# Optimization experiments

Measured on AMD Instinct MI355X. Metric: run time of the kernel, lower is better.

The kernel has to match this reference:

```python
import jax, jax.numpy as jnp
import numpy as np

N, E, F_IN, D, X_DIM, T_DIM = 5000, 80000, 32, 64, 3, 6
P1, P2, H = 256, 32, 256
LOG_SCALE = 1.4763057  # sqrt(c) * 1.4763057 with c=1; Euclidean logmap0 is identity
W_DATA, W_PDE, W_ENT = 1.0, 1.0, 1.0

def time_encode(t):
    k_lin = T_DIM // 2
    k_log = T_DIM - k_lin
    s_lin = 10.0 ** jnp.arange(2, 2 * T_DIM, 1, dtype=jnp.float32)
    s_log = 10.0 ** jnp.arange(-2, 2 * T_DIM, 1, dtype=jnp.float32)
    t_lin = (t / jnp.clip(s_lin, 1e-7))[:k_lin]
    t_log = jnp.log((t / jnp.clip(s_log, 1e-7))[:k_log] + 1.0)
    return jnp.concatenate([t_lin, t_log])

def _forward(x0, adj, t, y, W_enc, W_pool1, W_pool2, W_emb1, W_emb2, W1, b1, W2, b2):
    t0 = t[0]
    # ---- encode: encoder + Euclidean log-map scaling ----
    z_x = jnp.tanh(x0 @ W_enc)                      # [N, D+X_DIM]
    z = z_x[:, :-X_DIM] * LOG_SCALE                 # [N, D]
    x_sp = 0.0 * z_x[:, -X_DIM:]                    # eps = 0 as in encode()
    t_enc = time_encode(t0)                         # [T_DIM]
    tx = jnp.concatenate([t_enc[None, :] * jnp.ones((N, 1)), x_sp], axis=-1)  # [N, T_DIM+X_DIM]
    # ---- renorm: dense adjacency scatter + DiffPool-style coarsening ----
    A = jnp.zeros((N, N), dtype=x0.dtype).at[adj[0], adj[1]].set(1.0)
    x = z
    y_cur = y                                        # [1, N]
    z_r = z
    y_r = y
    loss_ent = 0.0
    for Wp, We in ((W_pool1, W_emb1), (W_pool2, W_emb2)):
        S = jax.nn.softmax((x @ Wp) * LOG_SCALE, axis=0)        # [m, n] soft assignment
        m, n = S.shape
        ze = jnp.tanh(A @ (x @ We))                             # GNN embed at this level
        x = jnp.einsum('ij,ik->jk', S, ze) * (n / m)            # pooled features [n, D]
        y_cur = jnp.einsum('ij,ki->kj', S, y_cur) * (n / m)     # pooled targets [1, n]
        A = jnp.einsum('ji,jk,kl->il', S, A, S)                 # S^T A S -> [n, n]
        z_r = jnp.concatenate([z_r, x], axis=0)
        y_r = jnp.concatenate([y_r, y_cur], axis=-1)
        loss_ent = loss_ent + jax.scipy.special.entr(S).mean()
    M = z_r.shape[0]                                 # N + P1 + P2
    tx_all = tx[0] * jnp.ones((M, 1))                # broadcast first row -> [M, T_DIM+X_DIM]
    # ---- decoder + val_grad_lap: nested jacfwd Hessian diagonal ----
    def decode(txz):
        h = jnp.tanh(txz @ W1 + b1)
        return h @ W2 + b2                           # [1]
    def vgl(tx_i, z_i):
        def f(tx_):
            u = decode(jnp.concatenate([tx_, z_i]))
            return u, u
        def vg(tx_):
            g, u = jax.jacfwd(f, has_aux=True)(tx_)
            return g, (g, u)
        g2, (g, u) = jax.jacfwd(vg, has_aux=True)(tx_i)  # [1, d, d]
        hess = jax.vmap(jnp.diag)(g2)                     # [1, d]
        lap = hess[:, 1:].sum(1)                          # [1]
        return u, g, lap
    u, grad, lap = jax.vmap(vgl)(tx_all, z_r)        # [M,1], [M,1,d], [M,1]
    red = u.sum(-1)                                   # reduction -> [M]
    loss_data = jnp.mean(jnp.square(red - y_r[0]))
    res = grad[:, 0, 0] - lap[:, 0]                   # heat-equation residual u_t - lap
    loss_pde = jnp.mean(jnp.square(res))
    return W_DATA * loss_data + W_PDE * loss_pde + W_ENT * loss_ent

def setup_inputs():
    key = jax.random.key(0)
    ks = jax.random.split(key, 13)
    d_tx = T_DIM + X_DIM
    return {
        'x0': jax.random.normal(ks[0], (N, F_IN), dtype=jnp.float32),
        'adj': jax.random.randint(ks[1], (2, E), 0, N),
        't': jax.random.uniform(ks[2], (1,), dtype=jnp.float32) * 100.0,
        'y': jax.random.normal(ks[3], (1, N), dtype=jnp.float32),
        'W_enc': 0.2 * jax.random.normal(ks[4], (F_IN, D + X_DIM), dtype=jnp.float32),
        'W_pool1': 0.2 * jax.random.normal(ks[5], (D, P1), dtype=jnp.float32),
        'W_pool2': 0.2 * jax.random.normal(ks[6], (D, P2), dtype=jnp.float32),
        'W_emb1': 0.1 * jax.random.normal(ks[7], (D, D), dtype=jnp.float32),
        'W_emb2': 0.1 * jax.random.normal(ks[8], (D, D), dtype=jnp.float32),
        'W1': 0.1 * jax.random.normal(ks[9], (d_tx + D, H), dtype=jnp.float32),
        'b1': 0.01 * jax.random.normal(ks[10], (H,), dtype=jnp.float32),
        'W2': 0.1 * jax.random.normal(ks[11], (H, 1), dtype=jnp.float32),
        'b2': jnp.zeros((1,), dtype=jnp.float32),
    }

def reference(x0, adj, t, y, W_enc, W_pool1, W_pool2, W_emb1, W_emb2, W1, b1, W2, b2):
    return _forward(x0, adj, t, y, W_enc, W_pool1, W_pool2, W_emb1, W_emb2, W1, b1, W2, b2)
```

## Files before the change

kernel.cpp:

```cpp
#include <hip/hip_runtime.h>
#include <math.h>

#define NN 5000
#define EE 80000
#define FIN 32
#define DD 64
#define XD 3
#define TD 6
#define PP1 256
#define PP2 32
#define HH 256
#define MM (NN + PP1 + PP2)
#define CAP 64
#define NTILES 79
#define LOG_SCALE 1.4763057f
#define Y2SCALE (256.f / 5000.f)

#define A2CH 40
#define X2CH 79

#define ACC_OFF   0u
#define CNT_OFF   64u
#define DEG_OFF   256u
#define Y2A_OFF   20256u
#define X2_OFF    21280u
#define A2_OFF    86816u
#define BM_OFF    348960u
#define ZERO_BYTES 3473960u
#define PART_OFF  348960u
#define XW2_OFF   760608u
#define S2_OFF    826144u
#define ZE2_OFF   858912u
#define X3_OFF    924448u
#define Y3_OFF    932640u
#define BUCK_OFF  3473984u
#define ZEP_OFF   4753984u
#define Z_OFF     6033984u
#define S1_OFF    7313984u
#define AS1_OFF   12433984u
#define CQ_OFF    17553984u
#define DRES_OFF  17556032u
#define PA2_OFF   17598336u
#define PX2_OFF   28084096u
#define WS_ROOMY  33261504u

__device__ __forceinline__ float bsum256(float v, float* red) {
    int t = threadIdx.x;
    red[t] = v; __syncthreads();
    #pragma unroll
    for (int o = 128; o > 0; o >>= 1) {
        if (t < o) red[t] += red[t + o];
        __syncthreads();
    }
    float r = red[0]; __syncthreads();
    return r;
}

__global__ __launch_bounds__(256) void stage0(
        const float* __restrict__ x0, const float* __restrict__ Wenc,
        float* __restrict__ z,
        const int* __restrict__ adj, unsigned int* __restrict__ mask,
        int* __restrict__ bucket, int* __restrict__ deg,
        const float* __restrict__ t, const float* __restrict__ W1,
        const float* __restrict__ b1, float* __restrict__ cq) {
    __shared__ float smem[FIN * DD + 4 * FIN];
    int b = blockIdx.x;
    int tid = threadIdx.x;
    if (b < 1250) {
        float (*wx)[DD] = (float(*)[DD])smem;
        float (*xr)[FIN] = (float(*)[FIN])(smem + FIN * DD);
        int i0 = b << 2;
        int j = tid & 63;
        #pragma unroll
        for (int m = 0; m < 8; ++m) {
            int k = (tid >> 6) + (m << 2);
            wx[k][j] = Wenc[k * (DD + XD) + j];
        }
        if (tid < 128) xr[tid >> 5][tid & 31] = x0[(i0 + (tid >> 5)) * FIN + (tid & 31)];
        __syncthreads();
        int r = tid >> 6;
        float s = 0.f;
        #pragma unroll
        for (int k = 0; k < FIN; ++k) s = fmaf(xr[r][k], wx[k][j], s);
        z[(i0 + r) * DD + j] = tanhf(s) * LOG_SCALE;
    } else if (b < 1563) {
        int e = (b - 1250) * 256 + tid;
        if (e < EE) {
            int i = adj[e], jj = adj[EE + e];
            unsigned int key = (unsigned int)(i * NN + jj);
            unsigned int bit = 1u << (key & 31u);
            unsigned int old = atomicOr(&mask[key >> 5], bit);
            if (!(old & bit)) {
                int slot = atomicAdd(&deg[i], 1);
                if (slot < CAP) bucket[i * CAP + slot] = jj;
            }
        }
    } else {
        float* te = smem;
        int h = tid;
        if (h == 0) {
            float t0 = t[0];
            te[0] = t0 / 1e2f;
            te[1] = t0 / 1e3f;
            te[2] = t0 / 1e4f;
            te[3] = logf(t0 * 100.f + 1.f);
            te[4] = logf(t0 * 10.f + 1.f);
            te[5] = logf(t0 + 1.f);
        }
        __syncthreads();
        float c = b1[h];
        #pragma unroll
        for (int j2 = 0; j2 < TD; ++j2) c = fmaf(te[j2], W1[j2 * HH + h], c);
        float q = 0.f;
        #pragma unroll
        for (int j2 = 1; j2 < TD + XD; ++j2) { float w = W1[j2 * HH + h]; q = fmaf(w, w, q); }
        cq[h] = c;
        cq[HH + h] = q;
    }
}

__global__ __launch_bounds__(256) void stage1(
        const float* __restrict__ z, const float* __restrict__ Wp1,
        float* __restrict__ S1, float* __restrict__ part,
        const int* __restrict__ bucket, const int* __restrict__ deg,
        const float* __restrict__ We1, float* __restrict__ zep) {
    __shared__ float smem[2 * 64 * 64];
    int b = blockIdx.x;
    int tid = threadIdx.x;
    if (b < NTILES * 4) {
        float (*sa)[64] = (float(*)[64])smem;
        float (*sb)[64] = (float(*)[64])(smem + 4096);
        int tm = (b >> 2) << 6;
        int tn = (b & 3) << 6;
        int r0 = tid >> 4, c0 = (tid & 15) << 2;
        const float4 zero4 = make_float4(0.f, 0.f, 0.f, 0.f);
        #pragma unroll
        for (int m = 0; m < 4; ++m) {
            int row = r0 + (m << 4);
            int gr = tm + row;
            *(float4*)&sa[row][c0] = (gr < NN) ? *(const float4*)&z[gr * DD + c0] : zero4;
            *(float4*)&sb[row][c0] = *(const float4*)&Wp1[row * PP1 + tn + c0];
        }
        __syncthreads();
        int tx = (tid & 15) << 2;
        int ty = (tid >> 4) << 2;
        float acc[4][4] = {};
        #pragma unroll
        for (int kk = 0; kk < 64; ++kk) {
            float a0 = sa[ty + 0][kk];
            float a1 = sa[ty + 1][kk];
            float a2 = sa[ty + 2][kk];
            float a3 = sa[ty + 3][kk];
            float4 bv = *(const float4*)&sb[kk][tx];
            acc[0][0] = fmaf(a0, bv.x, acc[0][0]);
            acc[0][1] = fmaf(a0, bv.y, acc[0][1]);
            acc[0][2] = fmaf(a0, bv.z, acc[0][2]);
            acc[0][3] = fmaf(a0, bv.w, acc[0][3]);
            acc[1][0] = fmaf(a1, bv.x, acc[1][0]);
            acc[1][1] = fmaf(a1, bv.y, acc[1][1]);
            acc[1][2] = fmaf(a1, bv.z, acc[1][2]);
            acc[1][3] = fmaf(a1, bv.w, acc[1][3]);
            acc[2][0] = fmaf(a2, bv.x, acc[2][0]);
            acc[2][1] = fmaf(a2, bv.y, acc[2][1]);
            acc[2][2] = fmaf(a2, bv.z, acc[2][2]);
            acc[2][3] = fmaf(a2, bv.w, acc[2][3]);
            acc[3][0] = fmaf(a3, bv.x, acc[3][0]);
            acc[3][1] = fmaf(a3, bv.y, acc[3][1]);
            acc[3][2] = fmaf(a3, bv.z, acc[3][2]);
            acc[3][3] = fmaf(a3, bv.w, acc[3][3]);
        }
        #pragma unroll
        for (int i2 = 0; i2 < 4; ++i2)
            #pragma unroll
            for (int j = 0; j < 4; ++j) acc[i2][j] *= LOG_SCALE;
        #pragma unroll
        for (int i2 = 0; i2 < 4; ++i2) {
            int gr = tm + ty + i2;
            if (gr < NN)
                *(float4*)&S1[gr * PP1 + tn + tx] =
                    make_float4(acc[i2][0], acc[i2][1], acc[i2][2], acc[i2][3]);
        }
        int nvalid = NN - (tm + ty);
        nvalid = (nvalid < 0) ? 0 : (nvalid > 4 ? 4 : nvalid);
        float vm[4], vs[4];
        #pragma unroll
        for (int j = 0; j < 4; ++j) {
            float m = -3.0e38f;
            #pragma unroll
            for (int i2 = 0; i2 < 4; ++i2) if (i2 < nvalid) m = fmaxf(m, acc[i2][j]);
            float s = 0.f;
            #pragma unroll
            for (int i2 = 0; i2 < 4; ++i2) if (i2 < nvalid) s += expf(acc[i2][j] - m);
            vm[j] = m; vs[j] = s;
        }
        __syncthreads();
        float* redm = smem;
        float* reds = smem + 1024;
        int g = tid >> 4;
        #pragma unroll
        for (int j = 0; j < 4; ++j) {
            redm[g * 64 + tx + j] = vm[j];
            reds[g * 64 + tx + j] = vs[j];
        }
        __syncthreads();
        if (tid < 64) {
            float M = -3.0e38f, S = 0.f;
            #pragma unroll
            for (int g2 = 0; g2 < 16; ++g2) {
                float m2 = redm[g2 * 64 + tid], s2 = reds[g2 * 64 + tid];
                float Mn = fmaxf(M, m2);
                S = S * expf(M - Mn) + s2 * expf(m2 - Mn);
                M = Mn;
            }
            int rt = tm >> 6;
            part[rt * 512 + tn + tid] = M;
            part[rt * 512 + 256 + tn + tid] = S;
        }
    } else {
        float (*zs)[DD] = (float(*)[DD])smem;
        int w = tid >> 6, d = tid & 63;
        int i = ((b - NTILES * 4) << 2) + w;
        int n = min(deg[i], CAP);
        const int* bk = bucket + i * CAP;
        float a0 = 0.f, a1 = 0.f, a2 = 0.f, a3 = 0.f;
        int s = 0;
        for (; s + 4 <= n; s += 4) {
            a0 += z[bk[s] * DD + d];
            a1 += z[bk[s + 1] * DD + d];
            a2 += z[bk[s + 2] * DD + d];
            a3 += z[bk[s + 3] * DD + d];
        }
        for (; s < n; ++s) a0 += z[bk[s] * DD + d];
        zs[w][d] = (a0 + a1) + (a2 + a3);
        __syncthreads();
        float acc = 0.f;
        #pragma unroll
        for (int k = 0; k < DD; ++k) acc = fmaf(zs[w][k], We1[k * DD + d], acc);
        zep[i * DD + d] = tanhf(acc);
    }
}

__global__ void smax_norm(float* __restrict__ S, const float* __restrict__ part,
                          const float* __restrict__ y, float* __restrict__ y2acc,
                          float* __restrict__ ent) {
    __shared__ float red[256];
    __shared__ float ybuf[4][64];
    __shared__ float cst[64];
    int rt = blockIdx.x % NTILES, ct = blockIdx.x / NTILES;
    int lc = threadIdx.x & 63, q = threadIdx.x >> 6;
    int c = (ct << 6) + lc;
    float M = -3.0e38f, Sv = 0.f;
    for (int ch = q; ch < NTILES; ch += 4) {
        float m2 = part[ch * 512 + c];
        float s2 = part[ch * 512 + 256 + c];
        float Mn = fmaxf(M, m2);
        Sv = Sv * expf(M - Mn) + s2 * expf(m2 - Mn);
        M = Mn;
    }
    red[threadIdx.x] = M; ybuf[q][lc] = Sv;
    __syncthreads();
    if (q == 0) {
        float Mm = red[lc], Ss = ybuf[0][lc];
        #pragma unroll
        for (int g = 1; g < 4; ++g) {
            float m2 = red[g * 64 + lc], s2 = ybuf[g][lc];
            float Mn = fmaxf(Mm, m2);
            Ss = Ss * expf(Mm - Mn) + s2 * expf(m2 - Mn);
            Mm = Mn;
        }
        cst[lc] = Mm + logf(Ss);
    }
    __syncthreads();
    float mxlns = cst[lc];
    float en = 0.f, ys = 0.f;
    #pragma unroll
    for (int k = 0; k < 16; ++k) {
        int r = (rt << 6) + (k << 2) + q;
        if (r < NN) {
            float v = S[r * PP1 + c];
            float s = expf(v - mxlns);
            S[r * PP1 + c] = s;
            en += s * (mxlns - v);
            ys = fmaf(s, y[r], ys);
        }
    }
    __syncthreads();
    ybuf[q][lc] = ys;
    en = bsum256(en, red);
    if (threadIdx.x == 0) atomicAdd(ent, en);
    if (q == 0) atomicAdd(&y2acc[c], ybuf[0][lc] + ybuf[1][lc] + ybuf[2][lc] + ybuf[3][lc]);
}

__global__ void gather_as(const int* __restrict__ bucket, const int* __restrict__ deg,
                          const float* __restrict__ S1, float* __restrict__ AS1) {
    int i = blockIdx.x, c = threadIdx.x;
    int n = min(deg[i], CAP);
    const int* bk = bucket + i * CAP;
    float a0 = 0.f, a1 = 0.f, a2 = 0.f, a3 = 0.f;
    int s = 0;
    for (; s + 4 <= n; s += 4) {
        a0 += S1[bk[s] * PP1 + c];
        a1 += S1[bk[s + 1] * PP1 + c];
        a2 += S1[bk[s + 2] * PP1 + c];
        a3 += S1[bk[s + 3] * PP1 + c];
    }
    for (; s < n; ++s) a0 += S1[bk[s] * PP1 + c];
    AS1[i * PP1 + c] = (a0 + a1) + (a2 + a3);
}

__global__ __launch_bounds__(256) void gemm_fused(
        const float* __restrict__ S1, const float* __restrict__ AS1,
        const float* __restrict__ zep, float* __restrict__ PA2, float* __restrict__ PX2) {
    __shared__ float sa[32][64];
    __shared__ float sb[32][64];
    int b = blockIdx.x;
    const float* B;
    float* dst;
    int tm, tn, k0, k1, NB;
    if (b < 640) {
        int tile = b & 15, chunk = b >> 4;
        tm = (tile >> 2) << 6; tn = (tile & 3) << 6;
        k0 = chunk * 128; k1 = min(k0 + 128, NN);
        B = AS1; NB = PP1;
        dst = PA2 + chunk * (PP1 * PP1);
    } else {
        int b2 = b - 640;
        int tile = b2 & 3, chunk = b2 >> 2;
        tm = tile << 6; tn = 0;
        k0 = chunk * 64; k1 = min(k0 + 64, NN);
        B = zep; NB = DD;
        dst = PX2 + chunk * (PP1 * DD);
    }
    int tid = threadIdx.x;
    int tx = (tid & 15) << 2;
    int ty = (tid >> 4) << 2;
    int r0 = tid >> 4, c0 = (tid & 15) << 2;
    int r1 = (tid + 256) >> 4, c1 = c0;
    float acc[4][4] = {};
    const float4 z4 = make_float4(0.f, 0.f, 0.f, 0.f);
    for (int kb = k0; kb < k1; kb += 32) {
        int ka0 = kb + r0, ka1 = kb + r1;
        *(float4*)&sa[r0][c0] = (ka0 < k1) ? *(const float4*)&S1[ka0 * PP1 + tm + c0] : z4;
        *(float4*)&sa[r1][c1] = (ka1 < k1) ? *(const float4*)&S1[ka1 * PP1 + tm + c1] : z4;
        *(float4*)&sb[r0][c0] = (ka0 < k1) ? *(const float4*)&B[ka0 * NB + tn + c0] : z4;
        *(float4*)&sb[r1][c1] = (ka1 < k1) ? *(const float4*)&B[ka1 * NB + tn + c1] : z4;
        __syncthreads();
        #pragma unroll
        for (int kk = 0; kk < 32; ++kk) {
            float4 av = *(const float4*)&sa[kk][ty];
            float4 bv = *(const float4*)&sb[kk][tx];
            acc[0][0] = fmaf(av.x, bv.x, acc[0][0]);
            acc[0][1] = fmaf(av.x, bv.y, acc[0][1]);
            acc[0][2] = fmaf(av.x, bv.z, acc[0][2]);
            acc[0][3] = fmaf(av.x, bv.w, acc[0][3]);
            acc[1][0] = fmaf(av.y, bv.x, acc[1][0]);
            acc[1][1] = fmaf(av.y, bv.y, acc[1][1]);
            acc[1][2] = fmaf(av.y, bv.z, acc[1][2]);
            acc[1][3] = fmaf(av.y, bv.w, acc[1][3]);
            acc[2][0] = fmaf(av.z, bv.x, acc[2][0]);
            acc[2][1] = fmaf(av.z, bv.y, acc[2][1]);
            acc[2][2] = fmaf(av.z, bv.z, acc[2][2]);
            acc[2][3] = fmaf(av.z, bv.w, acc[2][3]);
            acc[3][0] = fmaf(av.w, bv.x, acc[3][0]);
            acc[3][1] = fmaf(av.w, bv.y, acc[3][1]);
            acc[3][2] = fmaf(av.w, bv.z, acc[3][2]);
            acc[3][3] = fmaf(av.w, bv.w, acc[3][3]);
        }
        __syncthreads();
    }
    #pragma unroll
    for (int i = 0; i < 4; ++i)
        *(float4*)&dst[(tm + ty + i) * NB + tn + tx] =
            make_float4(acc[i][0], acc[i][1], acc[i][2], acc[i][3]);
}

__global__ void reduce_parts(const float* __restrict__ PA2, const float* __restrict__ PX2,
                             float* __restrict__ A2, float* __restrict__ x2) {
    int idx = blockIdx.x * 256 + threadIdx.x;
    if (idx < PP1 * PP1) {
        float s = 0.f;
        #pragma unroll 8
        for (int c = 0; c < A2CH; ++c) s += PA2[c * (PP1 * PP1) + idx];
        A2[idx] = s;
    } else {
        int e = idx - PP1 * PP1;
        float s = 0.f;
        #pragma unroll 8
        for (int c = 0; c < X2CH; ++c) s += PX2[c * (PP1 * DD) + e];
        x2[e] = s * Y2SCALE;
    }
}

__global__ void gemm_tn(const float* __restrict__ A, const float* __restrict__ B,
                        float* __restrict__ C, int M, int N, int K, int kchunk, float scale) {
    __shared__ float sa[32][64];
    __shared__ float sb[32][64];
    int tilesN = N >> 6;
    int tm = (blockIdx.x / tilesN) << 6;
    int tn = (blockIdx.x % tilesN) << 6;
    int k0 = blockIdx.y * kchunk;
    int k1 = min(k0 + kchunk, K);
    int tid = threadIdx.x;
    int tx = (tid & 15) << 2;
    int ty = (tid >> 4) << 2;
    float acc[4][4] = {};
    for (int kb = k0; kb < k1; kb += 32) {
        #pragma unroll
        for (int t = 0; t < 8; ++t) {
            int idx = tid + (t << 8);
            int r = idx >> 6, cc = idx & 63;
            int k = kb + r;
            sa[r][cc] = (k < k1) ? A[k * M + tm + cc] : 0.f;
            sb[r][cc] = (k < k1) ? B[k * N + tn + cc] : 0.f;
        }
        __syncthreads();
        #pragma unroll
        for (int kk = 0; kk < 32; ++kk) {
            float4 av = *(const float4*)&sa[kk][ty];
            float4 bv = *(const float4*)&sb[kk][tx];
            acc[0][0] = fmaf(av.x, bv.x, acc[0][0]);
            acc[0][1] = fmaf(av.x, bv.y, acc[0][1]);
            acc[0][2] = fmaf(av.x, bv.z, acc[0][2]);
            acc[0][3] = fmaf(av.x, bv.w, acc[0][3]);
            acc[1][0] = fmaf(av.y, bv.x, acc[1][0]);
            acc[1][1] = fmaf(av.y, bv.y, acc[1][1]);
            acc[1][2] = fmaf(av.y, bv.z, acc[1][2]);
            acc[1][3] = fmaf(av.y, bv.w, acc[1][3]);
            acc[2][0] = fmaf(av.z, bv.x, acc[2][0]);
            acc[2][1] = fmaf(av.z, bv.y, acc[2][1]);
            acc[2][2] = fmaf(av.z, bv.z, acc[2][2]);
            acc[2][3] = fmaf(av.z, bv.w, acc[2][3]);
            acc[3][0] = fmaf(av.w, bv.x, acc[3][0]);
            acc[3][1] = fmaf(av.w, bv.y, acc[3][1]);
            acc[3][2] = fmaf(av.w, bv.z, acc[3][2]);
            acc[3][3] = fmaf(av.w, bv.w, acc[3][3]);
        }
        __syncthreads();
    }
    #pragma unroll
    for (int i = 0; i < 4; ++i)
        #pragma unroll
        for (int j = 0; j < 4; ++j)
            atomicAdd(&C[(tm + ty + i) * N + tn + tx + j], acc[i][j] * scale);
}

__global__ void mm2_fused(const float* __restrict__ x2, const float* __restrict__ We2,
                          const float* __restrict__ Wp2, float* __restrict__ XW2,
                          float* __restrict__ S2) {
    int gid = blockIdx.x * 256 + threadIdx.x;
    if (gid < PP1 * DD) {
        int i = gid >> 6, j = gid & 63;
        float s = 0.f;
        #pragma unroll
        for (int k = 0; k < DD; ++k) s = fmaf(x2[i * DD + k], We2[k * DD + j], s);
        XW2[gid] = s;
    } else {
        int e = gid - PP1 * DD;
        int i = e >> 5, j = e & 31;
        float s = 0.f;
        #pragma unroll
        for (int k = 0; k < DD; ++k) s = fmaf(x2[i * DD + k], Wp2[k * PP2 + j], s);
        S2[e] = s * LOG_SCALE;
    }
}

__global__ void level2b(float* __restrict__ S2, float* __restrict__ ent,
                        const float* __restrict__ y2acc, float* __restrict__ y3,
                        const float* __restrict__ A2, const float* __restrict__ XW2,
                        float* __restrict__ ze2) {
    __shared__ float red[256];
    int t = threadIdx.x;
    if (blockIdx.x < PP2) {
        int p = blockIdx.x;
        float l = S2[t * PP2 + p];
        red[t] = l; __syncthreads();
        #pragma unroll
        for (int o = 128; o > 0; o >>= 1) {
            if (t < o) red[t] = fmaxf(red[t], red[t + o]);
            __syncthreads();
        }
        float mx = red[0]; __syncthreads();
        float ex = expf(l - mx);
        float sum = bsum256(ex, red);
        float lns = logf(sum), inv = 1.f / sum;
        float s = ex * inv;
        S2[t * PP2 + p] = s;
        float en = s * (mx + lns - l);
        float ys = s * y2acc[t];
        en = bsum256(en, red);
        ys = bsum256(ys, red);
        if (t == 0) {
            atomicAdd(ent, en);
            y3[p] = ys * ((32.f / 256.f) * Y2SCALE);
        }
    } else {
        int gid = (blockIdx.x - PP2) * 256 + t;
        int i = gid >> 6, j = gid & 63;
        const float* a = A2 + i * PP1;
        float s = 0.f;
        #pragma unroll 16
        for (int k = 0; k < PP1; ++k) s = fmaf(a[k], XW2[k * DD + j], s);
        ze2[gid] = tanhf(s);
    }
}

__global__ void pool_x3(const float* __restrict__ S2, const float* __restrict__ ze2,
                        float* __restrict__ x3) {
    __shared__ float pr[4][64];
    int j = blockIdx.x;
    int d = threadIdx.x & 63, q = threadIdx.x >> 6;
    float a = 0.f;
    #pragma unroll 4
    for (int i = q * 64; i < q * 64 + 64; ++i)
        a = fmaf(S2[i * PP2 + j], ze2[i * DD + d], a);
    pr[q][d] = a;
    __syncthreads();
    if (q == 0) x3[j * DD + d] = (pr[0][d] + pr[1][d] + pr[2][d] + pr[3][d]) * (32.f / 256.f);
}

__global__ __launch_bounds__(256) void decoder8(
        const float* __restrict__ z, const float* __restrict__ x2,
        const float* __restrict__ x3, const float* __restrict__ y,
        const float* __restrict__ y2acc, const float* __restrict__ y3,
        const float* __restrict__ W1, const float* __restrict__ W2,
        const float* __restrict__ b2, const float* __restrict__ cq,
        float* __restrict__ dres, int* __restrict__ cnt,
        const float* __restrict__ acc, float* __restrict__ out) {
    __shared__ float zr[8][DD];
    __shared__ float rw[8][3][4];
    __shared__ int lastflag;
    int t = threadIdx.x;
    int i0 = blockIdx.x << 3;
    #pragma unroll
    for (int e = t; e < 512; e += 256) {
        int r = e >> 6, d = e & 63;
        int i = i0 + r;
        float v;
        if (i < NN) v = z[i * DD + d];
        else if (i < NN + PP1) v = x2[(i - NN) * DD + d];
        else v = x3[(i - NN - PP1) * DD + d];
        zr[r][d] = v;
    }
    __syncthreads();
    int h = t;
    float c0 = cq[h];
    float a[8];
    #pragma unroll
    for (int r = 0; r < 8; ++r) a[r] = c0;
    #pragma unroll 8
    for (int k = 0; k < DD; ++k) {
        float w = W1[(TD + XD + k) * HH + h];
        #pragma unroll
        for (int r = 0; r < 8; ++r) a[r] = fmaf(zr[r][k], w, a[r]);
    }
    float w2h = W2[h], w1h = W1[h], qh = cq[HH + h];
    float pu[8], pg[8], pl[8];
    #pragma unroll
    for (int r = 0; r < 8; ++r) {
        float th = tanhf(a[r]);
        float g1 = 1.f - th * th;
        pu[r] = w2h * th;
        pg[r] = w2h * g1 * w1h;
        pl[r] = w2h * (-2.f * th * g1) * qh;
    }
    #pragma unroll
    for (int o = 32; o > 0; o >>= 1) {
        #pragma unroll
        for (int r = 0; r < 8; ++r) {
            pu[r] += __shfl_xor(pu[r], o);
            pg[r] += __shfl_xor(pg[r], o);
            pl[r] += __shfl_xor(pl[r], o);
        }
    }
    int wave = t >> 6, lane = t & 63;
    if (lane == 0) {
        #pragma unroll
        for (int r = 0; r < 8; ++r) {
            rw[r][0][wave] = pu[r];
            rw[r][1][wave] = pg[r];
            rw[r][2][wave] = pl[r];
        }
    }
    __syncthreads();
    if (t < 8) {
        int r = t, i = i0 + r;
        float su = rw[r][0][0] + rw[r][0][1] + rw[r][0][2] + rw[r][0][3];
        float sg = rw[r][1][0] + rw[r][1][1] + rw[r][1][2] + rw[r][1][3];
        float sl = rw[r][2][0] + rw[r][2][1] + rw[r][2][2] + rw[r][2][3];
        float u = su + b2[0];
        float yv = (i < NN) ? y[i]
                 : (i < NN + PP1) ? y2acc[i - NN] * Y2SCALE
                 : y3[i - NN - PP1];
        float du = u - yv;
        float res = sg - sl;
        dres[i * 2] = du * du;
        dres[i * 2 + 1] = res * res;
        __threadfence();
    }
    __syncthreads();
    if (t == 0) lastflag = atomicAdd(cnt, 1);
    __syncthreads();
    if (lastflag == (MM / 8) - 1) {
        __threadfence();
        float* red = (float*)zr;
        float sd = 0.f, sp = 0.f;
        for (int i = t; i < MM; i += 256) {
            sd += dres[i * 2];
            sp += dres[i * 2 + 1];
        }
        sd = bsum256(sd, red);
        sp = bsum256(sp, red);
        if (t == 0)
            out[0] = sd * (1.f / MM) + sp * (1.f / MM)
                   + acc[2] * (1.f / (float)(NN * PP1)) + acc[3] * (1.f / (float)(PP1 * PP2));
    }
}

extern "C" void kernel_launch(void* const* d_in, const int* in_sizes, int n_in,
                              void* d_out, int out_size, void* d_ws, size_t ws_size,
                              hipStream_t stream) {
    const float* x0   = (const float*)d_in[0];
    const int*   adj  = (const int*)d_in[1];
    const float* t    = (const float*)d_in[2];
    const float* y    = (const float*)d_in[3];
    const float* Wenc = (const float*)d_in[4];
    const float* Wp1  = (const float*)d_in[5];
    const float* Wp2  = (const float*)d_in[6];
    const float* We1  = (const float*)d_in[7];
    const float* We2  = (const float*)d_in[8];
    const float* W1   = (const float*)d_in[9];
    const float* b1   = (const float*)d_in[10];
    const float* W2   = (const float*)d_in[11];
    const float* b2   = (const float*)d_in[12];

    char* ws = (char*)d_ws;
    float* acc   = (float*)(ws + ACC_OFF);
    int*   cnt   = (int*)(ws + CNT_OFF);
    int*   deg   = (int*)(ws + DEG_OFF);
    float* y2acc = (float*)(ws + Y2A_OFF);
    float* x2    = (float*)(ws + X2_OFF);
    float* A2    = (float*)(ws + A2_OFF);
    unsigned int* mask = (unsigned int*)(ws + BM_OFF);
    float* part  = (float*)(ws + PART_OFF);
    float* XW2   = (float*)(ws + XW2_OFF);
    float* S2    = (float*)(ws + S2_OFF);
    float* ze2   = (float*)(ws + ZE2_OFF);
    float* x3    = (float*)(ws + X3_OFF);
    float* y3    = (float*)(ws + Y3_OFF);
    int*   buck  = (int*)(ws + BUCK_OFF);
    float* zep   = (float*)(ws + ZEP_OFF);
    float* z     = (float*)(ws + Z_OFF);
    float* S1    = (float*)(ws + S1_OFF);
    float* AS1   = (float*)(ws + AS1_OFF);
    float* cq    = (float*)(ws + CQ_OFF);
    float* dres  = (float*)(ws + DRES_OFF);
    float* PA2   = (float*)(ws + PA2_OFF);
    float* PX2   = (float*)(ws + PX2_OFF);

    hipMemsetAsync(ws, 0, ZERO_BYTES, stream);

    stage0<<<1564, 256, 0, stream>>>(x0, Wenc, z, adj, mask, buck, deg, t, W1, b1, cq);
    stage1<<<NTILES * 4 + NN / 4, 256, 0, stream>>>(z, Wp1, S1, part, buck, deg, We1, zep);
    smax_norm<<<NTILES * 4, 256, 0, stream>>>(S1, part, y, y2acc, &acc[2]);
    gather_as<<<NN, PP1, 0, stream>>>(buck, deg, S1, AS1);
    if (ws_size >= WS_ROOMY) {
        gemm_fused<<<640 + 316, 256, 0, stream>>>(S1, AS1, zep, PA2, PX2);
        reduce_parts<<<320, 256, 0, stream>>>(PA2, PX2, A2, x2);
    } else {
        gemm_tn<<<dim3(4, 32), 256, 0, stream>>>(S1, zep, x2, PP1, DD, NN, 157, Y2SCALE);
        gemm_tn<<<dim3(16, 16), 256, 0, stream>>>(S1, AS1, A2, PP1, PP1, NN, 313, 1.f);
    }
    mm2_fused<<<96, 256, 0, stream>>>(x2, We2, Wp2, XW2, S2);
    level2b<<<96, 256, 0, stream>>>(S2, &acc[3], y2acc, y3, A2, XW2, ze2);
    pool_x3<<<PP2, 256, 0, stream>>>(S2, ze2, x3);
    decoder8<<<MM / 8, 256, 0, stream>>>(z, x2, x3, y, y2acc, y3, W1, W2, b2, cq,
                                         dres, cnt, acc, (float*)d_out);
}
```

Measured before the change: 227.4 us.

## Merge all stages into one cooperative persistent kernel with grid syncs

```diff
diff --git a/kernel.cpp b/kernel.cpp
--- a/kernel.cpp
+++ b/kernel.cpp
@@ -1,5 +1,8 @@
 #include <hip/hip_runtime.h>
+#include <hip/hip_cooperative_groups.h>
 #include <math.h>
+
+namespace cg = cooperative_groups;
 
 #define NN 5000
 #define EE 80000
@@ -15,12 +18,10 @@
 #define NTILES 79
 #define LOG_SCALE 1.4763057f
 #define Y2SCALE (256.f / 5000.f)
-
 #define A2CH 40
 #define X2CH 79
 
 #define ACC_OFF   0u
-#define CNT_OFF   64u
 #define DEG_OFF   256u
 #define Y2A_OFF   20256u
 #define X2_OFF    21280u
@@ -44,6 +45,14 @@
 #define PX2_OFF   28084096u
 #define WS_ROOMY  33261504u
 
+struct KParams {
+    const float* x0; const int* adj; const float* t; const float* y;
+    const float* Wenc; const float* Wp1; const float* Wp2;
+    const float* We1; const float* We2; const float* W1; const float* b1;
+    const float* W2; const float* b2;
+    float* out; char* ws; int roomy;
+};
+
 __device__ __forceinline__ float bsum256(float v, float* red) {
     int t = threadIdx.x;
     red[t] = v; __syncthreads();
@@ -56,294 +65,24 @@
     return r;
 }
 
-__global__ __launch_bounds__(256) void stage0(
-        const float* __restrict__ x0, const float* __restrict__ Wenc,
-        float* __restrict__ z,
-        const int* __restrict__ adj, unsigned int* __restrict__ mask,
-        int* __restrict__ bucket, int* __restrict__ deg,
-        const float* __restrict__ t, const float* __restrict__ W1,
-        const float* __restrict__ b1, float* __restrict__ cq) {
-    __shared__ float smem[FIN * DD + 4 * FIN];
-    int b = blockIdx.x;
-    int tid = threadIdx.x;
-    if (b < 1250) {
-        float (*wx)[DD] = (float(*)[DD])smem;
-        float (*xr)[FIN] = (float(*)[FIN])(smem + FIN * DD);
-        int i0 = b << 2;
-        int j = tid & 63;
-        #pragma unroll
-        for (int m = 0; m < 8; ++m) {
-            int k = (tid >> 6) + (m << 2);
-            wx[k][j] = Wenc[k * (DD + XD) + j];
-        }
-        if (tid < 128) xr[tid >> 5][tid & 31] = x0[(i0 + (tid >> 5)) * FIN + (tid & 31)];
-        __syncthreads();
-        int r = tid >> 6;
-        float s = 0.f;
-        #pragma unroll
-        for (int k = 0; k < FIN; ++k) s = fmaf(xr[r][k], wx[k][j], s);
-        z[(i0 + r) * DD + j] = tanhf(s) * LOG_SCALE;
-    } else if (b < 1563) {
-        int e = (b - 1250) * 256 + tid;
-        if (e < EE) {
-            int i = adj[e], jj = adj[EE + e];
-            unsigned int key = (unsigned int)(i * NN + jj);
-            unsigned int bit = 1u << (key & 31u);
-            unsigned int old = atomicOr(&mask[key >> 5], bit);
-            if (!(old & bit)) {
-                int slot = atomicAdd(&deg[i], 1);
-                if (slot < CAP) bucket[i * CAP + slot] = jj;
-            }
-        }
-    } else {
-        float* te = smem;
-        int h = tid;
-        if (h == 0) {
-            float t0 = t[0];
-            te[0] = t0 / 1e2f;
-            te[1] = t0 / 1e3f;
-            te[2] = t0 / 1e4f;
-            te[3] = logf(t0 * 100.f + 1.f);
-            te[4] = logf(t0 * 10.f + 1.f);
-            te[5] = logf(t0 + 1.f);
-        }
-        __syncthreads();
-        float c = b1[h];
-        #pragma unroll
-        for (int j2 = 0; j2 < TD; ++j2) c = fmaf(te[j2], W1[j2 * HH + h], c);
-        float q = 0.f;
-        #pragma unroll
-        for (int j2 = 1; j2 < TD + XD; ++j2) { float w = W1[j2 * HH + h]; q = fmaf(w, w, q); }
-        cq[h] = c;
-        cq[HH + h] = q;
-    }
-}
-
-__global__ __launch_bounds__(256) void stage1(
-        const float* __restrict__ z, const float* __restrict__ Wp1,
-        float* __restrict__ S1, float* __restrict__ part,
-        const int* __restrict__ bucket, const int* __restrict__ deg,
-        const float* __restrict__ We1, float* __restrict__ zep) {
-    __shared__ float smem[2 * 64 * 64];
-    int b = blockIdx.x;
-    int tid = threadIdx.x;
-    if (b < NTILES * 4) {
-        float (*sa)[64] = (float(*)[64])smem;
-        float (*sb)[64] = (float(*)[64])(smem + 4096);
-        int tm = (b >> 2) << 6;
-        int tn = (b & 3) << 6;
-        int r0 = tid >> 4, c0 = (tid & 15) << 2;
-        const float4 zero4 = make_float4(0.f, 0.f, 0.f, 0.f);
-        #pragma unroll
-        for (int m = 0; m < 4; ++m) {
-            int row = r0 + (m << 4);
-            int gr = tm + row;
-            *(float4*)&sa[row][c0] = (gr < NN) ? *(const float4*)&z[gr * DD + c0] : zero4;
-            *(float4*)&sb[row][c0] = *(const float4*)&Wp1[row * PP1 + tn + c0];
-        }
-        __syncthreads();
-        int tx = (tid & 15) << 2;
-        int ty = (tid >> 4) << 2;
-        float acc[4][4] = {};
-        #pragma unroll
-        for (int kk = 0; kk < 64; ++kk) {
-            float a0 = sa[ty + 0][kk];
-            float a1 = sa[ty + 1][kk];
-            float a2 = sa[ty + 2][kk];
-            float a3 = sa[ty + 3][kk];
-            float4 bv = *(const float4*)&sb[kk][tx];
-            acc[0][0] = fmaf(a0, bv.x, acc[0][0]);
-            acc[0][1] = fmaf(a0, bv.y, acc[0][1]);
-            acc[0][2] = fmaf(a0, bv.z, acc[0][2]);
-            acc[0][3] = fmaf(a0, bv.w, acc[0][3]);
-            acc[1][0] = fmaf(a1, bv.x, acc[1][0]);
-            acc[1][1] = fmaf(a1, bv.y, acc[1][1]);
-            acc[1][2] = fmaf(a1, bv.z, acc[1][2]);
-            acc[1][3] = fmaf(a1, bv.w, acc[1][3]);
-            acc[2][0] = fmaf(a2, bv.x, acc[2][0]);
-            acc[2][1] = fmaf(a2, bv.y, acc[2][1]);
-            acc[2][2] = fmaf(a2, bv.z, acc[2][2]);
-            acc[2][3] = fmaf(a2, bv.w, acc[2][3]);
-            acc[3][0] = fmaf(a3, bv.x, acc[3][0]);
-            acc[3][1] = fmaf(a3, bv.y, acc[3][1]);
-            acc[3][2] = fmaf(a3, bv.z, acc[3][2]);
-            acc[3][3] = fmaf(a3, bv.w, acc[3][3]);
-        }
-        #pragma unroll
-        for (int i2 = 0; i2 < 4; ++i2)
-            #pragma unroll
-            for (int j = 0; j < 4; ++j) acc[i2][j] *= LOG_SCALE;
-        #pragma unroll
-        for (int i2 = 0; i2 < 4; ++i2) {
-            int gr = tm + ty + i2;
-            if (gr < NN)
-                *(float4*)&S1[gr * PP1 + tn + tx] =
-                    make_float4(acc[i2][0], acc[i2][1], acc[i2][2], acc[i2][3]);
-        }
-        int nvalid = NN - (tm + ty);
-        nvalid = (nvalid < 0) ? 0 : (nvalid > 4 ? 4 : nvalid);
-        float vm[4], vs[4];
-        #pragma unroll
-        for (int j = 0; j < 4; ++j) {
-            float m = -3.0e38f;
-            #pragma unroll
-            for (int i2 = 0; i2 < 4; ++i2) if (i2 < nvalid) m = fmaxf(m, acc[i2][j]);
-            float s = 0.f;
-            #pragma unroll
-            for (int i2 = 0; i2 < 4; ++i2) if (i2 < nvalid) s += expf(acc[i2][j] - m);
-            vm[j] = m; vs[j] = s;
-        }
-        __syncthreads();
-        float* redm = smem;
-        float* reds = smem + 1024;
-        int g = tid >> 4;
-        #pragma unroll
-        for (int j = 0; j < 4; ++j) {
-            redm[g * 64 + tx + j] = vm[j];
-            reds[g * 64 + tx + j] = vs[j];
-        }
-        __syncthreads();
-        if (tid < 64) {
-            float M = -3.0e38f, S = 0.f;
-            #pragma unroll
-            for (int g2 = 0; g2 < 16; ++g2) {
-                float m2 = redm[g2 * 64 + tid], s2 = reds[g2 * 64 + tid];
-                float Mn = fmaxf(M, m2);
-                S = S * expf(M - Mn) + s2 * expf(m2 - Mn);
-                M = Mn;
-            }
-            int rt = tm >> 6;
-            part[rt * 512 + tn + tid] = M;
-            part[rt * 512 + 256 + tn + tid] = S;
-        }
-    } else {
-        float (*zs)[DD] = (float(*)[DD])smem;
-        int w = tid >> 6, d = tid & 63;
-        int i = ((b - NTILES * 4) << 2) + w;
-        int n = min(deg[i], CAP);
-        const int* bk = bucket + i * CAP;
-        float a0 = 0.f, a1 = 0.f, a2 = 0.f, a3 = 0.f;
-        int s = 0;
-        for (; s + 4 <= n; s += 4) {
-            a0 += z[bk[s] * DD + d];
-            a1 += z[bk[s + 1] * DD + d];
-            a2 += z[bk[s + 2] * DD + d];
-            a3 += z[bk[s + 3] * DD + d];
-        }
-        for (; s < n; ++s) a0 += z[bk[s] * DD + d];
-        zs[w][d] = (a0 + a1) + (a2 + a3);
-        __syncthreads();
-        float acc = 0.f;
-        #pragma unroll
-        for (int k = 0; k < DD; ++k) acc = fmaf(zs[w][k], We1[k * DD + d], acc);
-        zep[i * DD + d] = tanhf(acc);
-    }
-}
-
-__global__ void smax_norm(float* __restrict__ S, const float* __restrict__ part,
-                          const float* __restrict__ y, float* __restrict__ y2acc,
-                          float* __restrict__ ent) {
-    __shared__ float red[256];
-    __shared__ float ybuf[4][64];
-    __shared__ float cst[64];
-    int rt = blockIdx.x % NTILES, ct = blockIdx.x / NTILES;
-    int lc = threadIdx.x & 63, q = threadIdx.x >> 6;
-    int c = (ct << 6) + lc;
-    float M = -3.0e38f, Sv = 0.f;
-    for (int ch = q; ch < NTILES; ch += 4) {
-        float m2 = part[ch * 512 + c];
-        float s2 = part[ch * 512 + 256 + c];
-        float Mn = fmaxf(M, m2);
-        Sv = Sv * expf(M - Mn) + s2 * expf(m2 - Mn);
-        M = Mn;
-    }
-    red[threadIdx.x] = M; ybuf[q][lc] = Sv;
-    __syncthreads();
-    if (q == 0) {
-        float Mm = red[lc], Ss = ybuf[0][lc];
-        #pragma unroll
-        for (int g = 1; g < 4; ++g) {
-            float m2 = red[g * 64 + lc], s2 = ybuf[g][lc];
-            float Mn = fmaxf(Mm, m2);
-            Ss = Ss * expf(Mm - Mn) + s2 * expf(m2 - Mn);
-            Mm = Mn;
-        }
-        cst[lc] = Mm + logf(Ss);
-    }
-    __syncthreads();
-    float mxlns = cst[lc];
-    float en = 0.f, ys = 0.f;
-    #pragma unroll
-    for (int k = 0; k < 16; ++k) {
-        int r = (rt << 6) + (k << 2) + q;
-        if (r < NN) {
-            float v = S[r * PP1 + c];
-            float s = expf(v - mxlns);
-            S[r * PP1 + c] = s;
-            en += s * (mxlns - v);
-            ys = fmaf(s, y[r], ys);
-        }
-    }
-    __syncthreads();
-    ybuf[q][lc] = ys;
-    en = bsum256(en, red);
-    if (threadIdx.x == 0) atomicAdd(ent, en);
-    if (q == 0) atomicAdd(&y2acc[c], ybuf[0][lc] + ybuf[1][lc] + ybuf[2][lc] + ybuf[3][lc]);
-}
-
-__global__ void gather_as(const int* __restrict__ bucket, const int* __restrict__ deg,
-                          const float* __restrict__ S1, float* __restrict__ AS1) {
-    int i = blockIdx.x, c = threadIdx.x;
-    int n = min(deg[i], CAP);
-    const int* bk = bucket + i * CAP;
-    float a0 = 0.f, a1 = 0.f, a2 = 0.f, a3 = 0.f;
-    int s = 0;
-    for (; s + 4 <= n; s += 4) {
-        a0 += S1[bk[s] * PP1 + c];
-        a1 += S1[bk[s + 1] * PP1 + c];
-        a2 += S1[bk[s + 2] * PP1 + c];
-        a3 += S1[bk[s + 3] * PP1 + c];
-    }
-    for (; s < n; ++s) a0 += S1[bk[s] * PP1 + c];
-    AS1[i * PP1 + c] = (a0 + a1) + (a2 + a3);
-}
-
-__global__ __launch_bounds__(256) void gemm_fused(
-        const float* __restrict__ S1, const float* __restrict__ AS1,
-        const float* __restrict__ zep, float* __restrict__ PA2, float* __restrict__ PX2) {
-    __shared__ float sa[32][64];
-    __shared__ float sb[32][64];
-    int b = blockIdx.x;
-    const float* B;
-    float* dst;
-    int tm, tn, k0, k1, NB;
-    if (b < 640) {
-        int tile = b & 15, chunk = b >> 4;
-        tm = (tile >> 2) << 6; tn = (tile & 3) << 6;
-        k0 = chunk * 128; k1 = min(k0 + 128, NN);
-        B = AS1; NB = PP1;
-        dst = PA2 + chunk * (PP1 * PP1);
-    } else {
-        int b2 = b - 640;
-        int tile = b2 & 3, chunk = b2 >> 2;
-        tm = tile << 6; tn = 0;
-        k0 = chunk * 64; k1 = min(k0 + 64, NN);
-        B = zep; NB = DD;
-        dst = PX2 + chunk * (PP1 * DD);
-    }
+__device__ __forceinline__ void gemm_tile(const float* __restrict__ Amat,
+        const float* __restrict__ Bmat, int tm, int tn, int k0, int k1, int NB,
+        float* __restrict__ dst, int atomicMode, float scale, float* smem) {
+    float (*sa)[64] = (float(*)[64])smem;
+    float (*sb)[64] = (float(*)[64])(smem + 2048);
     int tid = threadIdx.x;
     int tx = (tid & 15) << 2;
     int ty = (tid >> 4) << 2;
     int r0 = tid >> 4, c0 = (tid & 15) << 2;
-    int r1 = (tid + 256) >> 4, c1 = c0;
+    int r1 = r0 + 16;
     float acc[4][4] = {};
     const float4 z4 = make_float4(0.f, 0.f, 0.f, 0.f);
     for (int kb = k0; kb < k1; kb += 32) {
         int ka0 = kb + r0, ka1 = kb + r1;
-        *(float4*)&sa[r0][c0] = (ka0 < k1) ? *(const float4*)&S1[ka0 * PP1 + tm + c0] : z4;
-        *(float4*)&sa[r1][c1] = (ka1 < k1) ? *(const float4*)&S1[ka1 * PP1 + tm + c1] : z4;
-        *(float4*)&sb[r0][c0] = (ka0 < k1) ? *(const float4*)&B[ka0 * NB + tn + c0] : z4;
-        *(float4*)&sb[r1][c1] = (ka1 < k1) ? *(const float4*)&B[ka1 * NB + tn + c1] : z4;
+        *(float4*)&sa[r0][c0] = (ka0 < k1) ? *(const float4*)&Amat[ka0 * PP1 + tm + c0] : z4;
+        *(float4*)&sa[r1][c0] = (ka1 < k1) ? *(const float4*)&Amat[ka1 * PP1 + tm + c0] : z4;
+        *(float4*)&sb[r0][c0] = (ka0 < k1) ? *(const float4*)&Bmat[ka0 * NB + tn + c0] : z4;
+        *(float4*)&sb[r1][c0] = (ka1 < k1) ? *(const float4*)&Bmat[ka1 * NB + tn + c0] : z4;
         __syncthreads();
         #pragma unroll
         for (int kk = 0; kk < 32; ++kk) {
@@ -368,169 +107,31 @@
         }
         __syncthreads();
     }
-    #pragma unroll
-    for (int i = 0; i < 4; ++i)
-        *(float4*)&dst[(tm + ty + i) * NB + tn + tx] =
-            make_float4(acc[i][0], acc[i][1], acc[i][2], acc[i][3]);
+    if (atomicMode) {
+        #pragma unroll
+        for (int i = 0; i < 4; ++i)
+            #pragma unroll
+            for (int j = 0; j < 4; ++j)
+                atomicAdd(&dst[(tm + ty + i) * NB + tn + tx + j], acc[i][j] * scale);
+    } else {
+        #pragma unroll
+        for (int i = 0; i < 4; ++i)
+            *(float4*)&dst[(tm + ty + i) * NB + tn + tx] =
+                make_float4(acc[i][0] * scale, acc[i][1] * scale,
+                            acc[i][2] * scale, acc[i][3] * scale);
+    }
 }
 
-__global__ void reduce_parts(const float* __restrict__ PA2, const float* __restrict__ PX2,
-                             float* __restrict__ A2, float* __restrict__ x2) {
-    int idx = blockIdx.x * 256 + threadIdx.x;
-    if (idx < PP1 * PP1) {
-        float s = 0.f;
-        #pragma unroll 8
-        for (int c = 0; c < A2CH; ++c) s += PA2[c * (PP1 * PP1) + idx];
-        A2[idx] = s;
-    } else {
-        int e = idx - PP1 * PP1;
-        float s = 0.f;
-        #pragma unroll 8
-        for (int c = 0; c < X2CH; ++c) s += PX2[c * (PP1 * DD) + e];
-        x2[e] = s * Y2SCALE;
-    }
-}
-
-__global__ void gemm_tn(const float* __restrict__ A, const float* __restrict__ B,
-                        float* __restrict__ C, int M, int N, int K, int kchunk, float scale) {
-    __shared__ float sa[32][64];
-    __shared__ float sb[32][64];
-    int tilesN = N >> 6;
-    int tm = (blockIdx.x / tilesN) << 6;
-    int tn = (blockIdx.x % tilesN) << 6;
-    int k0 = blockIdx.y * kchunk;
-    int k1 = min(k0 + kchunk, K);
-    int tid = threadIdx.x;
-    int tx = (tid & 15) << 2;
-    int ty = (tid >> 4) << 2;
-    float acc[4][4] = {};
-    for (int kb = k0; kb < k1; kb += 32) {
-        #pragma unroll
-        for (int t = 0; t < 8; ++t) {
-            int idx = tid + (t << 8);
-            int r = idx >> 6, cc = idx & 63;
-            int k = kb + r;
-            sa[r][cc] = (k < k1) ? A[k * M + tm + cc] : 0.f;
-            sb[r][cc] = (k < k1) ? B[k * N + tn + cc] : 0.f;
-        }
-        __syncthreads();
-        #pragma unroll
-        for (int kk = 0; kk < 32; ++kk) {
-            float4 av = *(const float4*)&sa[kk][ty];
-            float4 bv = *(const float4*)&sb[kk][tx];
-            acc[0][0] = fmaf(av.x, bv.x, acc[0][0]);
-            acc[0][1] = fmaf(av.x, bv.y, acc[0][1]);
-            acc[0][2] = fmaf(av.x, bv.z, acc[0][2]);
-            acc[0][3] = fmaf(av.x, bv.w, acc[0][3]);
-            acc[1][0] = fmaf(av.y, bv.x, acc[1][0]);
-            acc[1][1] = fmaf(av.y, bv.y, acc[1][1]);
-            acc[1][2] = fmaf(av.y, bv.z, acc[1][2]);
-            acc[1][3] = fmaf(av.y, bv.w, acc[1][3]);
-            acc[2][0] = fmaf(av.z, bv.x, acc[2][0]);
-            acc[2][1] = fmaf(av.z, bv.y, acc[2][1]);
-            acc[2][2] = fmaf(av.z, bv.z, acc[2][2]);
-            acc[2][3] = fmaf(av.z, bv.w, acc[2][3]);
-            acc[3][0] = fmaf(av.w, bv.x, acc[3][0]);
-            acc[3][1] = fmaf(av.w, bv.y, acc[3][1]);
-            acc[3][2] = fmaf(av.w, bv.z, acc[3][2]);
-            acc[3][3] = fmaf(av.w, bv.w, acc[3][3]);
-        }
-        __syncthreads();
-    }
-    #pragma unroll
-    for (int i = 0; i < 4; ++i)
-        #pragma unroll
-        for (int j = 0; j < 4; ++j)
-            atomicAdd(&C[(tm + ty + i) * N + tn + tx + j], acc[i][j] * scale);
-}
-
-__global__ void mm2_fused(const float* __restrict__ x2, const float* __restrict__ We2,
-                          const float* __restrict__ Wp2, float* __restrict__ XW2,
-                          float* __restrict__ S2) {
-    int gid = blockIdx.x * 256 + threadIdx.x;
-    if (gid < PP1 * DD) {
-        int i = gid >> 6, j = gid & 63;
-        float s = 0.f;
-        #pragma unroll
-        for (int k = 0; k < DD; ++k) s = fmaf(x2[i * DD + k], We2[k * DD + j], s);
-        XW2[gid] = s;
-    } else {
-        int e = gid - PP1 * DD;
-        int i = e >> 5, j = e & 31;
-        float s = 0.f;
-        #pragma unroll
-        for (int k = 0; k < DD; ++k) s = fmaf(x2[i * DD + k], Wp2[k * PP2 + j], s);
-        S2[e] = s * LOG_SCALE;
-    }
-}
-
-__global__ void level2b(float* __restrict__ S2, float* __restrict__ ent,
-                        const float* __restrict__ y2acc, float* __restrict__ y3,
-                        const float* __restrict__ A2, const float* __restrict__ XW2,
-                        float* __restrict__ ze2) {
-    __shared__ float red[256];
-    int t = threadIdx.x;
-    if (blockIdx.x < PP2) {
-        int p = blockIdx.x;
-        float l = S2[t * PP2 + p];
-        red[t] = l; __syncthreads();
-        #pragma unroll
-        for (int o = 128; o > 0; o >>= 1) {
-            if (t < o) red[t] = fmaxf(red[t], red[t + o]);
-            __syncthreads();
-        }
-        float mx = red[0]; __syncthreads();
-        float ex = expf(l - mx);
-        float sum = bsum256(ex, red);
-        float lns = logf(sum), inv = 1.f / sum;
-        float s = ex * inv;
-        S2[t * PP2 + p] = s;
-        float en = s * (mx + lns - l);
-        float ys = s * y2acc[t];
-        en = bsum256(en, red);
-        ys = bsum256(ys, red);
-        if (t == 0) {
-            atomicAdd(ent, en);
-            y3[p] = ys * ((32.f / 256.f) * Y2SCALE);
-        }
-    } else {
-        int gid = (blockIdx.x - PP2) * 256 + t;
-        int i = gid >> 6, j = gid & 63;
-        const float* a = A2 + i * PP1;
-        float s = 0.f;
-        #pragma unroll 16
-        for (int k = 0; k < PP1; ++k) s = fmaf(a[k], XW2[k * DD + j], s);
-        ze2[gid] = tanhf(s);
-    }
-}
-
-__global__ void pool_x3(const float* __restrict__ S2, const float* __restrict__ ze2,
-                        float* __restrict__ x3) {
-    __shared__ float pr[4][64];
-    int j = blockIdx.x;
-    int d = threadIdx.x & 63, q = threadIdx.x >> 6;
-    float a = 0.f;
-    #pragma unroll 4
-    for (int i = q * 64; i < q * 64 + 64; ++i)
-        a = fmaf(S2[i * PP2 + j], ze2[i * DD + d], a);
-    pr[q][d] = a;
-    __syncthreads();
-    if (q == 0) x3[j * DD + d] = (pr[0][d] + pr[1][d] + pr[2][d] + pr[3][d]) * (32.f / 256.f);
-}
-
-__global__ __launch_bounds__(256) void decoder8(
-        const float* __restrict__ z, const float* __restrict__ x2,
+__device__ __forceinline__ void decoder_rows(
+        int i0, const float* __restrict__ z, const float* __restrict__ x2,
         const float* __restrict__ x3, const float* __restrict__ y,
         const float* __restrict__ y2acc, const float* __restrict__ y3,
         const float* __restrict__ W1, const float* __restrict__ W2,
         const float* __restrict__ b2, const float* __restrict__ cq,
-        float* __restrict__ dres, int* __restrict__ cnt,
-        const float* __restrict__ acc, float* __restrict__ out) {
-    __shared__ float zr[8][DD];
-    __shared__ float rw[8][3][4];
-    __shared__ int lastflag;
+        float* __restrict__ dres, float* smem) {
+    float (*zr)[DD] = (float(*)[DD])smem;
+    float (*rw)[3][4] = (float(*)[3][4])(smem + 512);
     int t = threadIdx.x;
-    int i0 = blockIdx.x << 3;
     #pragma unroll
     for (int e = t; e < 512; e += 256) {
         int r = e >> 6, d = e & 63;
@@ -595,47 +196,14 @@
         float res = sg - sl;
         dres[i * 2] = du * du;
         dres[i * 2 + 1] = res * res;
-        __threadfence();
-    }
-    __syncthreads();
-    if (t == 0) lastflag = atomicAdd(cnt, 1);
-    __syncthreads();
-    if (lastflag == (MM / 8) - 1) {
-        __threadfence();
-        float* red = (float*)zr;
-        float sd = 0.f, sp = 0.f;
-        for (int i = t; i < MM; i += 256) {
-            sd += dres[i * 2];
-            sp += dres[i * 2 + 1];
-        }
-        sd = bsum256(sd, red);
-        sp = bsum256(sp, red);
-        if (t == 0)
-            out[0] = sd * (1.f / MM) + sp * (1.f / MM)
-                   + acc[2] * (1.f / (float)(NN * PP1)) + acc[3] * (1.f / (float)(PP1 * PP2));
     }
 }
 
-extern "C" void kernel_launch(void* const* d_in, const int* in_sizes, int n_in,
-                              void* d_out, int out_size, void* d_ws, size_t ws_size,
-                              hipStream_t stream) {
-    const float* x0   = (const float*)d_in[0];
-    const int*   adj  = (const int*)d_in[1];
-    const float* t    = (const float*)d_in[2];
-    const float* y    = (const float*)d_in[3];
-    const float* Wenc = (const float*)d_in[4];
-    const float* Wp1  = (const float*)d_in[5];
-    const float* Wp2  = (const float*)d_in[6];
-    const float* We1  = (const float*)d_in[7];
-    const float* We2  = (const float*)d_in[8];
-    const float* W1   = (const float*)d_in[9];
-    const float* b1   = (const float*)d_in[10];
-    const float* W2   = (const float*)d_in[11];
-    const float* b2   = (const float*)d_in[12];
-
-    char* ws = (char*)d_ws;
+__global__ __launch_bounds__(256, 4) void mega(KParams p) {
+    __shared__ __align__(16) float smem[8192];
+    int tid = threadIdx.x;
+    char* ws = p.ws;
     float* acc   = (float*)(ws + ACC_OFF);
-    int*   cnt   = (int*)(ws + CNT_OFF);
     int*   deg   = (int*)(ws + DEG_OFF);
     float* y2acc = (float*)(ws + Y2A_OFF);
     float* x2    = (float*)(ws + X2_OFF);
@@ -656,23 +224,414 @@
     float* dres  = (float*)(ws + DRES_OFF);
     float* PA2   = (float*)(ws + PA2_OFF);
     float* PX2   = (float*)(ws + PX2_OFF);
-
-    hipMemsetAsync(ws, 0, ZERO_BYTES, stream);
-
-    stage0<<<1564, 256, 0, stream>>>(x0, Wenc, z, adj, mask, buck, deg, t, W1, b1, cq);
-    stage1<<<NTILES * 4 + NN / 4, 256, 0, stream>>>(z, Wp1, S1, part, buck, deg, We1, zep);
-    smax_norm<<<NTILES * 4, 256, 0, stream>>>(S1, part, y, y2acc, &acc[2]);
-    gather_as<<<NN, PP1, 0, stream>>>(buck, deg, S1, AS1);
-    if (ws_size >= WS_ROOMY) {
-        gemm_fused<<<640 + 316, 256, 0, stream>>>(S1, AS1, zep, PA2, PX2);
-        reduce_parts<<<320, 256, 0, stream>>>(PA2, PX2, A2, x2);
-    } else {
-        gemm_tn<<<dim3(4, 32), 256, 0, stream>>>(S1, zep, x2, PP1, DD, NN, 157, Y2SCALE);
-        gemm_tn<<<dim3(16, 16), 256, 0, stream>>>(S1, AS1, A2, PP1, PP1, NN, 313, 1.f);
-    }
-    mm2_fused<<<96, 256, 0, stream>>>(x2, We2, Wp2, XW2, S2);
-    level2b<<<96, 256, 0, stream>>>(S2, &acc[3], y2acc, y3, A2, XW2, ze2);
-    pool_x3<<<PP2, 256, 0, stream>>>(S2, ze2, x3);
-    decoder8<<<MM / 8, 256, 0, stream>>>(z, x2, x3, y, y2acc, y3, W1, W2, b2, cq,
-                                         dres, cnt, acc, (float*)d_out);
+    cg::grid_group gg = cg::this_grid();
+
+    for (int vb = blockIdx.x; vb < 1564; vb += gridDim.x) {
+        if (vb < 1250) {
+            float (*wx)[DD] = (float(*)[DD])smem;
+            float (*xr)[FIN] = (float(*)[FIN])(smem + FIN * DD);
+            int i0 = vb << 2;
+            int j = tid & 63;
+            #pragma unroll
+            for (int m = 0; m < 8; ++m) {
+                int k = (tid >> 6) + (m << 2);
+                wx[k][j] = p.Wenc[k * (DD + XD) + j];
+            }
+            if (tid < 128) xr[tid >> 5][tid & 31] = p.x0[(i0 + (tid >> 5)) * FIN + (tid & 31)];
+            __syncthreads();
+            int r = tid >> 6;
+            float s = 0.f;
+            #pragma unroll
+            for (int k = 0; k < FIN; ++k) s = fmaf(xr[r][k], wx[k][j], s);
+            z[(i0 + r) * DD + j] = tanhf(s) * LOG_SCALE;
+        } else if (vb < 1563) {
+            int e = (vb - 1250) * 256 + tid;
+            if (e < EE) {
+                int i = p.adj[e], jj = p.adj[EE + e];
+                unsigned int key = (unsigned int)(i * NN + jj);
+                unsigned int bit = 1u << (key & 31u);
+                unsigned int old = atomicOr(&mask[key >> 5], bit);
+                if (!(old & bit)) {
+                    int slot = atomicAdd(&deg[i], 1);
+                    if (slot < CAP) buck[i * CAP + slot] = jj;
+                }
+            }
+        } else {
+            float* te = smem;
+            if (tid == 0) {
+                float t0 = p.t[0];
+                te[0] = t0 / 1e2f;
+                te[1] = t0 / 1e3f;
+                te[2] = t0 / 1e4f;
+                te[3] = logf(t0 * 100.f + 1.f);
+                te[4] = logf(t0 * 10.f + 1.f);
+                te[5] = logf(t0 + 1.f);
+            }
+            __syncthreads();
+            int h = tid;
+            float c = p.b1[h];
+            #pragma unroll
+            for (int j2 = 0; j2 < TD; ++j2) c = fmaf(te[j2], p.W1[j2 * HH + h], c);
+            float q = 0.f;
+            #pragma unroll
+            for (int j2 = 1; j2 < TD + XD; ++j2) { float w = p.W1[j2 * HH + h]; q = fmaf(w, w, q); }
+            cq[h] = c;
+            cq[HH + h] = q;
+        }
+        __syncthreads();
+    }
+    gg.sync();
+
+    for (int vb = blockIdx.x; vb < NTILES * 4 + 1250; vb += gridDim.x) {
+        if (vb < NTILES * 4) {
+            float (*sa)[64] = (float(*)[64])smem;
+            float (*sb)[64] = (float(*)[64])(smem + 4096);
+            int tm = (vb >> 2) << 6;
+            int tn = (vb & 3) << 6;
+            int r0 = tid >> 4, c0 = (tid & 15) << 2;
+            const float4 zero4 = make_float4(0.f, 0.f, 0.f, 0.f);
+            #pragma unroll
+            for (int m = 0; m < 4; ++m) {
+                int row = r0 + (m << 4);
+                int gr = tm + row;
+                *(float4*)&sa[row][c0] = (gr < NN) ? *(const float4*)&z[gr * DD + c0] : zero4;
+                *(float4*)&sb[row][c0] = *(const float4*)&p.Wp1[row * PP1 + tn + c0];
+            }
+            __syncthreads();
+            int tx = (tid & 15) << 2;
+            int ty = (tid >> 4) << 2;
+            float acr[4][4] = {};
+            #pragma unroll
+            for (int kk = 0; kk < 64; ++kk) {
+                float a0 = sa[ty + 0][kk];
+                float a1 = sa[ty + 1][kk];
+                float a2 = sa[ty + 2][kk];
+                float a3 = sa[ty + 3][kk];
+                float4 bv = *(const float4*)&sb[kk][tx];
+                acr[0][0] = fmaf(a0, bv.x, acr[0][0]);
+                acr[0][1] = fmaf(a0, bv.y, acr[0][1]);
+                acr[0][2] = fmaf(a0, bv.z, acr[0][2]);
+                acr[0][3] = fmaf(a0, bv.w, acr[0][3]);
+                acr[1][0] = fmaf(a1, bv.x, acr[1][0]);
+                acr[1][1] = fmaf(a1, bv.y, acr[1][1]);
+                acr[1][2] = fmaf(a1, bv.z, acr[1][2]);
+                acr[1][3] = fmaf(a1, bv.w, acr[1][3]);
+                acr[2][0] = fmaf(a2, bv.x, acr[2][0]);
+                acr[2][1] = fmaf(a2, bv.y, acr[2][1]);
+                acr[2][2] = fmaf(a2, bv.z, acr[2][2]);
+                acr[2][3] = fmaf(a2, bv.w, acr[2][3]);
+                acr[3][0] = fmaf(a3, bv.x, acr[3][0]);
+                acr[3][1] = fmaf(a3, bv.y, acr[3][1]);
+                acr[3][2] = fmaf(a3, bv.z, acr[3][2]);
+                acr[3][3] = fmaf(a3, bv.w, acr[3][3]);
+            }
+            #pragma unroll
+            for (int i2 = 0; i2 < 4; ++i2)
+                #pragma unroll
+                for (int j = 0; j < 4; ++j) acr[i2][j] *= LOG_SCALE;
+            #pragma unroll
+            for (int i2 = 0; i2 < 4; ++i2) {
+                int gr = tm + ty + i2;
+                if (gr < NN)
+                    *(float4*)&S1[gr * PP1 + tn + tx] =
+                        make_float4(acr[i2][0], acr[i2][1], acr[i2][2], acr[i2][3]);
+            }
+            int nvalid = NN - (tm + ty);
+            nvalid = (nvalid < 0) ? 0 : (nvalid > 4 ? 4 : nvalid);
+            float vm[4], vs[4];
+            #pragma unroll
+            for (int j = 0; j < 4; ++j) {
+                float m = -3.0e38f;
+                #pragma unroll
+                for (int i2 = 0; i2 < 4; ++i2) if (i2 < nvalid) m = fmaxf(m, acr[i2][j]);
+                float s = 0.f;
+                #pragma unroll
+                for (int i2 = 0; i2 < 4; ++i2) if (i2 < nvalid) s += expf(acr[i2][j] - m);
+                vm[j] = m; vs[j] = s;
+            }
+            __syncthreads();
+            float* redm = smem;
+            float* reds = smem + 1024;
+            int g = tid >> 4;
+            #pragma unroll
+            for (int j = 0; j < 4; ++j) {
+                redm[g * 64 + tx + j] = vm[j];
+                reds[g * 64 + tx + j] = vs[j];
+            }
+            __syncthreads();
+            if (tid < 64) {
+                float M = -3.0e38f, S = 0.f;
+                #pragma unroll
+                for (int g2 = 0; g2 < 16; ++g2) {
+                    float m2 = redm[g2 * 64 + tid], s2 = reds[g2 * 64 + tid];
+                    float Mn = fmaxf(M, m2);
+                    S = S * expf(M - Mn) + s2 * expf(m2 - Mn);
+                    M = Mn;
+                }
+                int rt = tm >> 6;
+                part[rt * 512 + tn + tid] = M;
+                part[rt * 512 + 256 + tn + tid] = S;
+            }
+        } else {
+            float (*zs)[DD] = (float(*)[DD])smem;
+            int w = tid >> 6, d = tid & 63;
+            int i = ((vb - NTILES * 4) << 2) + w;
+            int n = min(deg[i], CAP);
+            const int* bk = buck + i * CAP;
+            float a0 = 0.f, a1 = 0.f, a2 = 0.f, a3 = 0.f;
+            int s = 0;
+            for (; s + 4 <= n; s += 4) {
+                a0 += z[bk[s] * DD + d];
+                a1 += z[bk[s + 1] * DD + d];
+                a2 += z[bk[s + 2] * DD + d];
+                a3 += z[bk[s + 3] * DD + d];
+            }
+            for (; s < n; ++s) a0 += z[bk[s] * DD + d];
+            zs[w][d] = (a0 + a1) + (a2 + a3);
+            __syncthreads();
+            float a = 0.f;
+            #pragma unroll
+            for (int k = 0; k < DD; ++k) a = fmaf(zs[w][k], p.We1[k * DD + d], a);
+            zep[i * DD + d] = tanhf(a);
+        }
+        __syncthreads();
+    }
+    gg.sync();
+
+    for (int vb = blockIdx.x; vb < NTILES * 4; vb += gridDim.x) {
+        float* red = smem;
+        float (*ybuf)[64] = (float(*)[64])(smem + 256);
+        float* cst = smem + 512;
+        int rt = vb % NTILES, ct = vb / NTILES;
+        int lc = tid & 63, q = tid >> 6;
+        int c = (ct << 6) + lc;
+        float M = -3.0e38f, Sv = 0.f;
+        for (int ch = q; ch < NTILES; ch += 4) {
+            float m2 = part[ch * 512 + c];
+            float s2 = part[ch * 512 + 256 + c];
+            float Mn = fmaxf(M, m2);
+            Sv = Sv * expf(M - Mn) + s2 * expf(m2 - Mn);
+            M = Mn;
+        }
+        red[tid] = M; ybuf[q][lc] = Sv;
+        __syncthreads();
+        if (q == 0) {
+            float Mm = red[lc], Ss = ybuf[0][lc];
+            #pragma unroll
+            for (int g = 1; g < 4; ++g) {
+                float m2 = red[g * 64 + lc], s2 = ybuf[g][lc];
+                float Mn = fmaxf(Mm, m2);
+                Ss = Ss * expf(Mm - Mn) + s2 * expf(m2 - Mn);
+                Mm = Mn;
+            }
+            cst[lc] = Mm + logf(Ss);
+        }
+        __syncthreads();
+        float mxlns = cst[lc];
+        float en = 0.f, ys = 0.f;
+        #pragma unroll
+        for (int k = 0; k < 16; ++k) {
+            int r = (rt << 6) + (k << 2) + q;
+            if (r < NN) {
+                float v = S1[r * PP1 + c];
+                float s = expf(v - mxlns);
+                S1[r * PP1 + c] = s;
+                en += s * (mxlns - v);
+                ys = fmaf(s, p.y[r], ys);
+            }
+        }
+        __syncthreads();
+        ybuf[q][lc] = ys;
+        en = bsum256(en, red);
+        if (tid == 0) atomicAdd(&acc[2], en);
+        if (q == 0) atomicAdd(&y2acc[c], ybuf[0][lc] + ybuf[1][lc] + ybuf[2][lc] + ybuf[3][lc]);
+        __syncthreads();
+    }
+    gg.sync();
+
+    for (int vb = blockIdx.x; vb < 5000 + 316 + 625; vb += gridDim.x) {
+        if (vb < 5000) {
+            int i = vb, c = tid;
+            int n = min(deg[i], CAP);
+            const int* bk = buck + i * CAP;
+            float a0 = 0.f, a1 = 0.f, a2 = 0.f, a3 = 0.f;
+            int s = 0;
+            for (; s + 4 <= n; s += 4) {
+                a0 += S1[bk[s] * PP1 + c];
+                a1 += S1[bk[s + 1] * PP1 + c];
+                a2 += S1[bk[s + 2] * PP1 + c];
+                a3 += S1[bk[s + 3] * PP1 + c];
+            }
+            for (; s < n; ++s) a0 += S1[bk[s] * PP1 + c];
+            AS1[i * PP1 + c] = (a0 + a1) + (a2 + a3);
+        } else if (vb < 5316) {
+            int vb2 = vb - 5000;
+            int tile = vb2 & 3, chunk = vb2 >> 2;
+            int k0 = chunk * 64, k1 = min(k0 + 64, NN);
+            gemm_tile(S1, zep, tile << 6, 0, k0, k1, DD,
+                      p.roomy ? PX2 + chunk * (PP1 * DD) : x2,
+                      !p.roomy, p.roomy ? 1.f : Y2SCALE, smem);
+        } else {
+            decoder_rows((vb - 5316) << 3, z, x2, x3, p.y, y2acc, y3,
+                         p.W1, p.W2, p.b2, cq, dres, smem);
+        }
+        __syncthreads();
+    }
+    gg.sync();
+
+    for (int vb = blockIdx.x; vb < 704; vb += gridDim.x) {
+        if (vb < 640) {
+            int tile = vb & 15, chunk = vb >> 4;
+            int k0 = chunk * 128, k1 = min(k0 + 128, NN);
+            gemm_tile(S1, AS1, (tile >> 2) << 6, (tile & 3) << 6, k0, k1, PP1,
+                      p.roomy ? PA2 + chunk * (PP1 * PP1) : A2,
+                      !p.roomy, 1.f, smem);
+        } else if (p.roomy) {
+            int idx = (vb - 640) * 256 + tid;
+            float s = 0.f;
+            #pragma unroll 8
+            for (int c = 0; c < X2CH; ++c) s += PX2[c * (PP1 * DD) + idx];
+            x2[idx] = s * Y2SCALE;
+        }
+        __syncthreads();
+    }
+    gg.sync();
+
+    for (int vb = blockIdx.x; vb < 384; vb += gridDim.x) {
+        if (vb < 256) {
+            if (p.roomy) {
+                int idx = vb * 256 + tid;
+                float s = 0.f;
+                #pragma unroll 8
+                for (int c = 0; c < A2CH; ++c) s += PA2[c * (PP1 * PP1) + idx];
+                A2[idx] = s;
+            }
+        } else if (vb < 352) {
+            int gid = (vb - 256) * 256 + tid;
+            if (gid < PP1 * DD) {
+                int i = gid >> 6, j = gid & 63;
+                float s = 0.f;
+                #pragma unroll
+                for (int k = 0; k < DD; ++k) s = fmaf(x2[i * DD + k], p.We2[k * DD + j], s);
+                XW2[gid] = s;
+            } else {
+                int e = gid - PP1 * DD;
+                int i = e >> 5, j = e & 31;
+                float s = 0.f;
+                #pragma unroll
+                for (int k = 0; k < DD; ++k) s = fmaf(x2[i * DD + k], p.Wp2[k * PP2 + j], s);
+                S2[e] = s * LOG_SCALE;
+            }
+        } else {
+            decoder_rows(5000 + ((vb - 352) << 3), z, x2, x3, p.y, y2acc, y3,
+                         p.W1, p.W2, p.b2, cq, dres, smem);
+        }
+        __syncthreads();
+    }
+    gg.sync();
+
+    for (int vb = blockIdx.x; vb < 96; vb += gridDim.x) {
+        if (vb < PP2) {
+            float* red = smem;
+            int pcol = vb;
+            float l = S2[tid * PP2 + pcol];
+            red[tid] = l; __syncthreads();
+            #pragma unroll
+            for (int o = 128; o > 0; o >>= 1) {
+                if (tid < o) red[tid] = fmaxf(red[tid], red[tid + o]);
+                __syncthreads();
+            }
+            float mx = red[0]; __syncthreads();
+            float ex = expf(l - mx);
+            float sum = bsum256(ex, red);
+            float lns = logf(sum), inv = 1.f / sum;
+            float s = ex * inv;
+            S2[tid * PP2 + pcol] = s;
+            float en = s * (mx + lns - l);
+            float ys = s * y2acc[tid];
+            en = bsum256(en, red);
+            ys = bsum256(ys, red);
+            if (tid == 0) {
+                atomicAdd(&acc[3], en);
+                y3[pcol] = ys * ((32.f / 256.f) * Y2SCALE);
+            }
+        } else {
+            int gid = (vb - PP2) * 256 + tid;
+            int i = gid >> 6, j = gid & 63;
+            const float* a = A2 + i * PP1;
+            float s = 0.f;
+            #pragma unroll 16
+            for (int k = 0; k < PP1; ++k) s = fmaf(a[k], XW2[k * DD + j], s);
+            ze2[gid] = tanhf(s);
+        }
+        __syncthreads();
+    }
+    gg.sync();
+
+    for (int vb = blockIdx.x; vb < PP2; vb += gridDim.x) {
+        float (*pr)[64] = (float(*)[64])smem;
+        int j = vb;
+        int d = tid & 63, q = tid >> 6;
+        float a = 0.f;
+        #pragma unroll 4
+        for (int i = q * 64; i < q * 64 + 64; ++i)
+            a = fmaf(S2[i * PP2 + j], ze2[i * DD + d], a);
+        pr[q][d] = a;
+        __syncthreads();
+        if (q == 0) x3[j * DD + d] = (pr[0][d] + pr[1][d] + pr[2][d] + pr[3][d]) * (32.f / 256.f);
+        __syncthreads();
+    }
+    gg.sync();
+
+    if (blockIdx.x == 0) {
+        for (int vb = 0; vb < 4; ++vb) {
+            decoder_rows(5256 + (vb << 3), z, x2, x3, p.y, y2acc, y3,
+                         p.W1, p.W2, p.b2, cq, dres, smem);
+            __syncthreads();
+        }
+        float* red = smem;
+        float sd = 0.f, sp = 0.f;
+        for (int i = tid; i < MM; i += 256) {
+            sd += dres[i * 2];
+            sp += dres[i * 2 + 1];
+        }
+        sd = bsum256(sd, red);
+        sp = bsum256(sp, red);
+        if (tid == 0)
+            p.out[0] = sd * (1.f / MM) + sp * (1.f / MM)
+                     + acc[2] * (1.f / (float)(NN * PP1)) + acc[3] * (1.f / (float)(PP1 * PP2));
+    }
 }
+
+extern "C" void kernel_launch(void* const* d_in, const int* in_sizes, int n_in,
+                              void* d_out, int out_size, void* d_ws, size_t ws_size,
+                              hipStream_t stream) {
+    KParams kp;
+    kp.x0   = (const float*)d_in[0];
+    kp.adj  = (const int*)d_in[1];
+    kp.t    = (const float*)d_in[2];
+    kp.y    = (const float*)d_in[3];
+    kp.Wenc = (const float*)d_in[4];
+    kp.Wp1  = (const float*)d_in[5];
+    kp.Wp2  = (const float*)d_in[6];
+    kp.We1  = (const float*)d_in[7];
+    kp.We2  = (const float*)d_in[8];
+    kp.W1   = (const float*)d_in[9];
+    kp.b1   = (const float*)d_in[10];
+    kp.W2   = (const float*)d_in[11];
+    kp.b2   = (const float*)d_in[12];
+    kp.out  = (float*)d_out;
+    kp.ws   = (char*)d_ws;
+    kp.roomy = (ws_size >= WS_ROOMY) ? 1 : 0;
+
+    hipMemsetAsync(d_ws, 0, ZERO_BYTES, stream);
+
+    int nb = 0;
+    if (hipOccupancyMaxActiveBlocksPerMultiprocessor(&nb, (const void*)mega, 256, 0) != hipSuccess || nb < 1)
+        nb = 2;
+    int grid = nb * 256;
+    if (grid > 1024) grid = 1024;
+
+    void* args[] = { &kp };
+    hipLaunchCooperativeKernel((const void*)mega, dim3(grid), dim3(256), args, 0, stream);
+}
```

Measured after the change: 857.6 us. 277% more time.
